# Performance work log

Measured on AMD Instinct MI355X. Metric: run time of the kernel, lower is better.

Reference implementation:

```python
import jax, jax.numpy as jnp
import numpy as np
import math

H = 12
DH = 64
MAX_POS = 1024

def setup_inputs() -> dict:
    key = jax.random.key(0)
    ks = jax.random.split(key, 8)
    B, L, D = 2, 1024, 768
    s = 0.02
    return {
        "hidden_states": jax.random.normal(ks[0], (B, L, D), jnp.float32),
        "attention_mask": jnp.zeros((B, 1, 1, L), jnp.float32),
        "struct_matrix": jax.random.uniform(ks[1], (5, B, 1, L, L), jnp.float32),
        "Wq": jax.random.normal(ks[2], (D, D), jnp.float32) * s,
        "bq": jnp.zeros((D,), jnp.float32),
        "Wk": jax.random.normal(ks[3], (D, D), jnp.float32) * s,
        "bk": jnp.zeros((D,), jnp.float32),
        "Wv": jax.random.normal(ks[4], (D, D), jnp.float32) * s,
        "bv": jnp.zeros((D,), jnp.float32),
        "dist_emb": jax.random.normal(ks[5], (2 * MAX_POS - 1, DH), jnp.float32) * s,
        "ssan_w": jax.random.normal(ks[6], (5, H, DH, DH), jnp.float32) * s,
        "abs_bias": jnp.zeros((5, H), jnp.float32),
    }

def reference(hidden_states, attention_mask, struct_matrix, Wq, bq, Wk, bk, Wv, bv, dist_emb, ssan_w, abs_bias):
    B, L, D = hidden_states.shape

    def heads(x):  # [B,L,D] -> [B,H,L,dh]
        return x.reshape(B, L, H, DH).transpose(0, 2, 1, 3)

    q = heads(hidden_states @ Wq + bq)
    k = heads(hidden_states @ Wk + bk)
    v = heads(hidden_states @ Wv + bv)

    scores = jnp.einsum('bhqd,bhkd->bhqk', q, k)

    # relative_key_query positional scores
    pos_ids = jnp.arange(L)
    distance = pos_ids[:, None] - pos_ids[None, :]          # [L,L]
    pos = dist_emb[distance + MAX_POS - 1]                  # [L,L,dh]
    scores = scores + jnp.einsum('bhld,lrd->bhlr', q, pos)
    scores = scores + jnp.einsum('bhrd,lrd->bhlr', k, pos)

    scores = scores / math.sqrt(DH)
    scores = scores + attention_mask

    # 5 SSAN bilinear bias terms, masked by structural matrices
    for i in range(5):
        bias = jnp.einsum('bhqd,hde,bhke->bhqk', q, ssan_w[i], k)
        scores = scores + (bias + abs_bias[i][None, :, None, None]) * struct_matrix[i]

    probs = jax.nn.softmax(scores, axis=-1)
    ctx = jnp.einsum('bhqk,bhkd->bqhd', probs, v).reshape(B, L, D)
    return ctx
```

## Files before the change

kernel.cpp:

```cpp
#include <hip/hip_runtime.h>
#include <math.h>

#define NB 2
#define NL 1024
#define ND 768
#define NH 12
#define DH 64

typedef _Float16 f16;
typedef _Float16 f16x2 __attribute__((ext_vector_type(2)));
typedef _Float16 f16x4 __attribute__((ext_vector_type(4)));
typedef _Float16 f16x8 __attribute__((ext_vector_type(8)));
typedef float f32x4 __attribute__((ext_vector_type(4)));

#define MFMA16(a, b, c) __builtin_amdgcn_mfma_f32_16x16x32_f16((a), (b), (c), 0, 0, 0)

__device__ __forceinline__ void soft_barrier() {
    asm volatile("s_waitcnt lgkmcnt(0)\n\ts_barrier" ::: "memory");
}

__global__ __launch_bounds__(256) void prep_kernel(
    const float* __restrict__ Wq, const float* __restrict__ Wk,
    const float* __restrict__ Wv, const float* __restrict__ sw,
    const float* __restrict__ de,
    f16* __restrict__ wt, f16* __restrict__ swt, f16* __restrict__ de16)
{
    __shared__ float sT[64 * 66];
    const int t = threadIdx.x;
    const int tile = blockIdx.x;

    if (tile >= 492) {
        const int base = (tile - 492) * 2048 + t * 8;
        if (base < 2047 * 64) {
            float4 a = *(const float4*)&de[base];
            float4 b = *(const float4*)&de[base + 4];
            f16x8 hv;
            hv[0] = (f16)a.x; hv[1] = (f16)a.y; hv[2] = (f16)a.z; hv[3] = (f16)a.w;
            hv[4] = (f16)b.x; hv[5] = (f16)b.y; hv[6] = (f16)b.z; hv[7] = (f16)b.w;
            *(f16x8*)&de16[base] = hv;
        }
        return;
    }

    const float* S; f16* D; int sRS, dRS;
    if (tile < 432) {
        const int mat = tile / 144, r2 = tile % 144, ht = r2 / 12, kt = r2 % 12;
        const float* W = (mat == 0) ? Wq : (mat == 1) ? Wk : Wv;
        S = W + (size_t)(kt * 64) * ND + ht * 64;
        D = wt + (size_t)((mat * NH + ht) * 64) * ND + kt * 64;
        sRS = ND; dRS = ND;
    } else {
        const int i = tile - 432;
        S = sw + (size_t)i * 4096;
        D = swt + (size_t)i * 4096;
        sRS = 64; dRS = 64;
    }

    {
        const int kk = t >> 2, nb = (t & 3) * 16;
        float v[16];
        #pragma unroll
        for (int j = 0; j < 4; ++j)
            *(float4*)&v[4 * j] = *(const float4*)&S[(size_t)kk * sRS + nb + 4 * j];
        #pragma unroll
        for (int jj = 0; jj < 16; ++jj)
            sT[(nb + jj) * 66 + kk] = v[jj];
    }
    soft_barrier();
    {
        const int n = t >> 2, kb = (t & 3) * 16;
        f16 tmp[16];
        #pragma unroll
        for (int j = 0; j < 8; ++j) {
            float2 x = *(float2*)&sT[n * 66 + kb + 2 * j];
            tmp[2 * j]     = (f16)x.x;
            tmp[2 * j + 1] = (f16)x.y;
        }
        *(f16x8*)&D[(size_t)n * dRS + kb]     = *(f16x8*)&tmp[0];
        *(f16x8*)&D[(size_t)n * dRS + kb + 8] = *(f16x8*)&tmp[8];
    }
}

__global__ __launch_bounds__(256, 4) void qkv_kernel(
    const float* __restrict__ hs, const f16* __restrict__ wt,
    const float* __restrict__ bq, const float* __restrict__ bk,
    const float* __restrict__ bv,
    f16* __restrict__ qf, f16* __restrict__ kf, f16* __restrict__ vt)
{
    __shared__ f16 sA[64 * 72], sB[64 * 72];
    __shared__ float sT[64 * 66];

    const int m0  = blockIdx.x * 64;
    const int y   = blockIdx.y;
    const int mat = y / NH, h = y % NH;
    const int t = threadIdx.x, lane = t & 63, w = t >> 6;
    const int quad = lane >> 4, l15 = lane & 15;
    const int wm = w >> 1, wn = w & 1;

    const float* bias = (mat == 0) ? bq : (mat == 1) ? bk : bv;

    f32x4 acc[2][2];
    #pragma unroll
    for (int r = 0; r < 2; ++r)
        #pragma unroll
        for (int c = 0; c < 2; ++c) acc[r][c] = (f32x4){0.f, 0.f, 0.f, 0.f};

    const int srow = t >> 2, scol = (t & 3) * 16;
    const float* Ag = hs + (size_t)(m0 + srow) * ND + scol;
    const f16* Bg = wt + ((size_t)y * 64 + srow) * ND + scol;

    for (int k0 = 0; k0 < ND; k0 += 64) {
        soft_barrier();
        {
            float4 a0 = *(const float4*)&Ag[k0];
            float4 a1 = *(const float4*)&Ag[k0 + 4];
            float4 a2 = *(const float4*)&Ag[k0 + 8];
            float4 a3 = *(const float4*)&Ag[k0 + 12];
            f16x8 ha, hb;
            ha[0] = (f16)a0.x; ha[1] = (f16)a0.y; ha[2] = (f16)a0.z; ha[3] = (f16)a0.w;
            ha[4] = (f16)a1.x; ha[5] = (f16)a1.y; ha[6] = (f16)a1.z; ha[7] = (f16)a1.w;
            hb[0] = (f16)a2.x; hb[1] = (f16)a2.y; hb[2] = (f16)a2.z; hb[3] = (f16)a2.w;
            hb[4] = (f16)a3.x; hb[5] = (f16)a3.y; hb[6] = (f16)a3.z; hb[7] = (f16)a3.w;
            *(f16x8*)&sA[srow * 72 + scol]     = ha;
            *(f16x8*)&sA[srow * 72 + scol + 8] = hb;
        }
        *(f16x8*)&sB[srow * 72 + scol]     = *(const f16x8*)&Bg[k0];
        *(f16x8*)&sB[srow * 72 + scol + 8] = *(const f16x8*)&Bg[k0 + 8];
        soft_barrier();
        #pragma unroll
        for (int kk = 0; kk < 64; kk += 32) {
            const int ko = kk + quad * 8;
            f16x8 a0 = *(f16x8*)&sA[(32 * wm + l15) * 72 + ko];
            f16x8 a1 = *(f16x8*)&sA[(32 * wm + 16 + l15) * 72 + ko];
            f16x8 b0 = *(f16x8*)&sB[(32 * wn + l15) * 72 + ko];
            f16x8 b1 = *(f16x8*)&sB[(32 * wn + 16 + l15) * 72 + ko];
            acc[0][0] = MFMA16(a0, b0, acc[0][0]);
            acc[0][1] = MFMA16(a0, b1, acc[0][1]);
            acc[1][0] = MFMA16(a1, b0, acc[1][0]);
            acc[1][1] = MFMA16(a1, b1, acc[1][1]);
        }
    }
    soft_barrier();

    const int bb = m0 >> 10;
    const int lbase = m0 & 1023;
    const int bh = bb * NH + h;

    if (mat < 2) {
        #pragma unroll
        for (int r = 0; r < 2; ++r)
            #pragma unroll
            for (int c = 0; c < 2; ++c) {
                const int col = 32 * wn + 16 * c + l15;
                const float bz = bias[h * 64 + col];
                #pragma unroll
                for (int rr = 0; rr < 4; ++rr)
                    sT[(32 * wm + 16 * r + 4 * quad + rr) * 66 + col] = acc[r][c][rr] + bz;
            }
        soft_barrier();
        const int orow = t >> 2, ocb = (t & 3) * 16;
        f16 tmp[16];
        #pragma unroll
        for (int j = 0; j < 8; ++j) {
            float2 x = *(float2*)&sT[orow * 66 + ocb + 2 * j];
            tmp[2 * j] = (f16)x.x; tmp[2 * j + 1] = (f16)x.y;
        }
        f16* dst = ((mat == 0) ? qf : kf) + ((size_t)bh * NL + lbase + orow) * DH + ocb;
        *(f16x8*)dst       = *(f16x8*)&tmp[0];
        *(f16x8*)(dst + 8) = *(f16x8*)&tmp[8];
    } else {
        #pragma unroll
        for (int r = 0; r < 2; ++r)
            #pragma unroll
            for (int c = 0; c < 2; ++c) {
                const int col = 32 * wn + 16 * c + l15;
                const float bz = bias[h * 64 + col];
                #pragma unroll
                for (int rr = 0; rr < 4; ++rr)
                    sT[col * 66 + 32 * wm + 16 * r + 4 * quad + rr] = acc[r][c][rr] + bz;
            }
        soft_barrier();
        const int d = t >> 2, lcb = (t & 3) * 16;
        f16 tmp[16];
        #pragma unroll
        for (int j = 0; j < 8; ++j) {
            float2 x = *(float2*)&sT[d * 66 + lcb + 2 * j];
            tmp[2 * j] = (f16)x.x; tmp[2 * j + 1] = (f16)x.y;
        }
        f16* dst = vt + ((size_t)bh * DH + d) * NL + lbase + lcb;
        *(f16x8*)dst       = *(f16x8*)&tmp[0];
        *(f16x8*)(dst + 8) = *(f16x8*)&tmp[8];
    }
}

__global__ __launch_bounds__(256, 2) void attn_kernel(
    const f16* __restrict__ qf, const f16* __restrict__ kf,
    const f16* __restrict__ vt, const f16* __restrict__ swt,
    const float* __restrict__ mask, const float* __restrict__ struct_m,
    const f16* __restrict__ de16, const float* __restrict__ abs_bias,
    float* __restrict__ out)
{
    __shared__ f16 sK[64 * 72];
    __shared__ f16 sVt[2][64 * 72];
    __shared__ f16 sE[96 * 72];
    __shared__ f16 sQEl[96 * 34];
    __shared__ f16 sKEl[96 * 34];
    __shared__ float sS[32 * 68];
    __shared__ f16 sP[32 * 72];
    __shared__ float sAlpha[32], sL[32];

    const int l0 = blockIdx.x * 32;
    const int bh = blockIdx.y;
    const int bb = bh / NH, h = bh % NH;
    const int t  = threadIdx.x;
    const int lane  = t & 63;
    const int w     = t >> 6;
    const int quad  = lane >> 4;
    const int l15   = lane & 15;
    const int msub  = w >> 1;
    const int npair = w & 1;

    f16x8 aQ[2], aW[5][2];
    {
        const size_t qrow = ((size_t)bh * NL + l0 + 16 * msub + l15) * DH;
        #pragma unroll
        for (int K = 0; K < 2; ++K)
            aQ[K] = *(const f16x8*)&qf[qrow + 32 * K + 8 * quad];
    }

    {
        #pragma unroll
        for (int b = 0; b < 2; ++b) {
            const int pb0  = (b == 0) ? 0 : 3;
            const int pcnt = (b == 0) ? 3 : 2;
            #pragma unroll
            for (int pi = 0; pi < 3; ++pi) {
                if (pi < pcnt) {
                    const int p = pb0 + pi;
                    const f16* Wp = swt + ((size_t)(p * NH + h)) * 64 * 64;
                    #pragma unroll
                    for (int ntl = 0; ntl < 2; ++ntl) {
                        const int nt = 2 * npair + ntl;
                        f32x4 c = (f32x4){0.f, 0.f, 0.f, 0.f};
                        #pragma unroll
                        for (int K = 0; K < 2; ++K) {
                            f16x8 bw = *(const f16x8*)&Wp[(size_t)(16 * nt + l15) * 64 + 32 * K + 8 * quad];
                            c = MFMA16(aQ[K], bw, c);
                        }
                        #pragma unroll
                        for (int r = 0; r < 4; ++r)
                            sE[(pi * 32 + 16 * msub + 4 * quad + r) * 72 + 16 * nt + l15] = (f16)c[r];
                    }
                }
            }
            soft_barrier();
            #pragma unroll
            for (int pi = 0; pi < 3; ++pi) {
                if (pi < pcnt) {
                    #pragma unroll
                    for (int K = 0; K < 2; ++K)
                        aW[pb0 + pi][K] =
                            *(const f16x8*)&sE[(pi * 32 + 16 * msub + l15) * 72 + 32 * K + 8 * quad];
                }
            }
            soft_barrier();
        }
    }

    float ab[5];
    #pragma unroll
    for (int p = 0; p < 5; ++p) ab[p] = abs_bias[p * NH + h];

    float pf_st[5][2][4], pf_mask[2];
    f16x8 kreg[2], vreg[2], ereg[3];

    auto issue_kv = [&](int r0s) {
        const int row = t >> 3, col = (t & 7) * 8;
        const f16* ks = kf + ((size_t)bh * NL + r0s) * DH;
        kreg[0] = *(const f16x8*)&ks[row * 64 + col];
        kreg[1] = *(const f16x8*)&ks[(row + 32) * 64 + col];
        const f16* vs = vt + (size_t)bh * DH * NL + r0s;
        vreg[0] = *(const f16x8*)&vs[(size_t)row * NL + col];
        vreg[1] = *(const f16x8*)&vs[(size_t)(row + 32) * NL + col];
    };
    auto write_kv = [&](int buf) {
        const int row = t >> 3, col = (t & 7) * 8;
        *(f16x8*)&sK[row * 72 + col]             = kreg[0];
        *(f16x8*)&sK[(row + 32) * 72 + col]      = kreg[1];
        *(f16x8*)&sVt[buf][row * 72 + col]       = vreg[0];
        *(f16x8*)&sVt[buf][(row + 32) * 72 + col] = vreg[1];
    };
    auto issue_E = [&](int r0s) {
        const int ebase = l0 - r0s + 960;
        #pragma unroll
        for (int p2 = 0; p2 < 3; ++p2) {
            const int idx = t + 256 * p2;
            const int er = idx >> 3, colE = (idx & 7) * 8;
            if (er < 95)
                ereg[p2] = *(const f16x8*)&de16[(size_t)(ebase + er) * DH + colE];
        }
    };
    auto write_E = [&]() {
        #pragma unroll
        for (int p2 = 0; p2 < 3; ++p2) {
            const int idx = t + 256 * p2;
            const int er = idx >> 3, colE = (idx & 7) * 8;
            if (er < 95)
                *(f16x8*)&sE[er * 72 + colE] = ereg[p2];
        }
    };
    auto prefetch = [&](int r0s) {
        #pragma unroll
        for (int n = 0; n < 2; ++n) {
            const int j = 32 * npair + 16 * n + l15;
            pf_mask[n] = mask[bb * NL + r0s + j];
            #pragma unroll
            for (int r = 0; r < 4; ++r) {
                const int i = 16 * msub + 4 * quad + r;
                #pragma unroll
                for (int p = 0; p < 5; ++p)
                    pf_st[p][n][r] =
                        struct_m[((size_t)(p * NB + bb) * NL + l0 + i) * NL + r0s + j];
            }
        }
    };

    issue_kv(0);
    issue_E(0);
    write_kv(0);
    write_E();
    prefetch(0);

    const int sm_i = t >> 3;
    const int sm_jb = t & 7;
    float m_cur = -INFINITY, l_cur = 0.f;
    f32x4 O[2];
    O[0] = (f32x4){0.f, 0.f, 0.f, 0.f};
    O[1] = (f32x4){0.f, 0.f, 0.f, 0.f};

    soft_barrier();

    for (int kt = 0; kt < 16; ++kt) {
        const int cur = kt & 1;

        {
            const int krow = (16 * w + l15) * 72;
            f16x8 ak0 = *(f16x8*)&sK[krow + quad * 8];
            f16x8 ak1 = *(f16x8*)&sK[krow + 32 + quad * 8];
            #pragma unroll
            for (int c = 0; c < 3; ++c) {
                const int nt = 3 - w + c;
                const int erow = (16 * nt + l15) * 72;
                f16x8 e0 = *(f16x8*)&sE[erow + quad * 8];
                f16x8 e1 = *(f16x8*)&sE[erow + 32 + quad * 8];
                f32x4 ck = (f32x4){0.f, 0.f, 0.f, 0.f};
                ck = MFMA16(ak0, e0, ck);
                ck = MFMA16(ak1, e1, ck);
                const int base = (16 * nt + l15) * 34 + 16 * w + 4 * quad;
                f16x2 lo = {(f16)ck[0], (f16)ck[1]};
                f16x2 hi = {(f16)ck[2], (f16)ck[3]};
                *(f16x2*)&sKEl[base]     = lo;
                *(f16x2*)&sKEl[base + 2] = hi;
            }
            const int qs = 3 * npair + msub;
            const int qc = 3 - npair;
            #pragma unroll
            for (int c = 0; c < 3; ++c) {
                if (c < qc) {
                    const int nt = qs + c;
                    const int erow = (16 * nt + l15) * 72;
                    f16x8 e0 = *(f16x8*)&sE[erow + quad * 8];
                    f16x8 e1 = *(f16x8*)&sE[erow + 32 + quad * 8];
                    f32x4 cq = (f32x4){0.f, 0.f, 0.f, 0.f};
                    cq = MFMA16(aQ[0], e0, cq);
                    cq = MFMA16(aQ[1], e1, cq);
                    const int base = (16 * nt + l15) * 34 + 16 * msub + 4 * quad;
                    f16x2 lo = {(f16)cq[0], (f16)cq[1]};
                    f16x2 hi = {(f16)cq[2], (f16)cq[3]};
                    *(f16x2*)&sQEl[base]     = lo;
                    *(f16x2*)&sQEl[base + 2] = hi;
                }
            }
        }
        soft_barrier();

        {
            if (kt < 15) {
                issue_kv((kt + 1) * 64);
                issue_E((kt + 1) * 64);
            }

            f32x4 acc[2][6];
            #pragma unroll
            for (int n = 0; n < 2; ++n)
                #pragma unroll
                for (int p = 0; p < 6; ++p)
                    acc[n][p] = (f32x4){0.f, 0.f, 0.f, 0.f};

            #pragma unroll
            for (int K = 0; K < 2; ++K) {
                const int koff = K * 32 + quad * 8;
                f16x8 bk2[2];
                #pragma unroll
                for (int n = 0; n < 2; ++n)
                    bk2[n] = *(f16x8*)&sK[(32 * npair + 16 * n + l15) * 72 + koff];
                #pragma unroll
                for (int n = 0; n < 2; ++n)
                    acc[n][0] = MFMA16(aQ[K], bk2[n], acc[n][0]);
                #pragma unroll
                for (int p = 0; p < 5; ++p)
                    #pragma unroll
                    for (int n = 0; n < 2; ++n)
                        acc[n][1 + p] = MFMA16(aW[p][K], bk2[n], acc[n][1 + p]);
            }

            #pragma unroll
            for (int n = 0; n < 2; ++n) {
                const int j = 32 * npair + 16 * n + l15;
                #pragma unroll
                for (int r = 0; r < 4; ++r) {
                    const int i = 16 * msub + 4 * quad + r;
                    const int tp = i - j + 63;
                    float posv = (float)sQEl[tp * 34 + i] + (float)sKEl[tp * 34 + j];
                    float s = (acc[n][0][r] + posv) * 0.125f + pf_mask[n];
                    #pragma unroll
                    for (int p = 0; p < 5; ++p)
                        s += (acc[n][1 + p][r] + ab[p]) * pf_st[p][n][r];
                    sS[i * 68 + j] = s;
                }
            }
        }
        soft_barrier();

        {
            float sv[8];
            float smax = -INFINITY;
            #pragma unroll
            for (int k = 0; k < 8; ++k) {
                sv[k] = sS[sm_i * 68 + sm_jb + 8 * k];
                smax = fmaxf(smax, sv[k]);
            }
            #pragma unroll
            for (int off = 4; off > 0; off >>= 1)
                smax = fmaxf(smax, __shfl_xor(smax, off, 8));
            const float m_new = fmaxf(m_cur, smax);
            const float alpha = __expf(m_cur - m_new);
            float rsum = 0.f;
            #pragma unroll
            for (int k = 0; k < 8; ++k) {
                float p = __expf(sv[k] - m_new);
                sP[sm_i * 72 + sm_jb + 8 * k] = (f16)p;
                rsum += p;
            }
            #pragma unroll
            for (int off = 4; off > 0; off >>= 1)
                rsum += __shfl_xor(rsum, off, 8);
            l_cur = l_cur * alpha + rsum;
            m_cur = m_new;
            if (sm_jb == 0) { sAlpha[sm_i] = alpha; sL[sm_i] = l_cur; }

            if (kt < 15) {
                write_kv(cur ^ 1);
                write_E();
                prefetch((kt + 1) * 64);
            }
        }
        soft_barrier();

        {
            float a4[4];
            #pragma unroll
            for (int r = 0; r < 4; ++r) a4[r] = sAlpha[16 * msub + 4 * quad + r];
            #pragma unroll
            for (int n = 0; n < 2; ++n)
                #pragma unroll
                for (int r = 0; r < 4; ++r) O[n][r] *= a4[r];

            const int prow = (16 * msub + l15) * 72;
            #pragma unroll
            for (int K = 0; K < 2; ++K) {
                const int koff = K * 32 + quad * 8;
                f16x8 pfr = *(f16x8*)&sP[prow + koff];
                #pragma unroll
                for (int n = 0; n < 2; ++n) {
                    f16x8 vfr = *(f16x8*)&sVt[cur][(32 * npair + 16 * n + l15) * 72 + koff];
                    O[n] = MFMA16(pfr, vfr, O[n]);
                }
            }
        }
    }

    float linv[4];
    #pragma unroll
    for (int r = 0; r < 4; ++r) linv[r] = 1.0f / sL[16 * msub + 4 * quad + r];
    #pragma unroll
    for (int n = 0; n < 2; ++n) {
        const int dh = 32 * npair + 16 * n + l15;
        #pragma unroll
        for (int r = 0; r < 4; ++r) {
            const int i = 16 * msub + 4 * quad + r;
            out[((size_t)bb * NL + l0 + i) * ND + h * DH + dh] = O[n][r] * linv[r];
        }
    }
}

extern "C" void kernel_launch(void* const* d_in, const int* in_sizes, int n_in,
                              void* d_out, int out_size, void* d_ws, size_t ws_size,
                              hipStream_t stream) {
    const float* hs   = (const float*)d_in[0];
    const float* mask = (const float*)d_in[1];
    const float* stm  = (const float*)d_in[2];
    const float* Wq   = (const float*)d_in[3];
    const float* bq   = (const float*)d_in[4];
    const float* Wk   = (const float*)d_in[5];
    const float* bk   = (const float*)d_in[6];
    const float* Wv   = (const float*)d_in[7];
    const float* bv   = (const float*)d_in[8];
    const float* de   = (const float*)d_in[9];
    const float* sw   = (const float*)d_in[10];
    const float* abb  = (const float*)d_in[11];
    float* outp = (float*)d_out;

    const size_t NQKV = (size_t)NB * NH * NL * DH;
    char* ws = (char*)d_ws;
    f16* qf   = (f16*)ws;                 ws += NQKV * 2;
    f16* kf   = (f16*)ws;                 ws += NQKV * 2;
    f16* vtb  = (f16*)ws;                 ws += NQKV * 2;
    f16* wt   = (f16*)ws;                 ws += (size_t)2304 * 768 * 2;
    f16* swt  = (f16*)ws;                 ws += (size_t)245760 * 2;
    f16* de16 = (f16*)ws;

    prep_kernel<<<556, 256, 0, stream>>>(Wq, Wk, Wv, sw, de, wt, swt, de16);
    qkv_kernel<<<dim3(32, 36), 256, 0, stream>>>(hs, wt, bq, bk, bv, qf, kf, vtb);
    attn_kernel<<<dim3(32, 24), 256, 0, stream>>>(qf, kf, vtb, swt,
                                                  mask, stm, de16, abb, outp);
}
```

Baseline: 220.0 us.

## Retile QKV GEMM to 128x128 with double-buffered LDS and pre-converted fp16 input

The hidden-states fp32-to-fp16 conversion moves into the prep kernel, so the QKV GEMM reads fp16 activations directly. The QKV kernel switches from 64x64 to 128x128 tiles with a 4x4 MFMA grid per wave, which raises data reuse. It also double-buffers LDS, prefetching the next K-slice into registers while computing the current one. The cost is higher register and LDS pressure, lower occupancy (launch bounds 2), a grid of only 288 blocks, and an extra fp16 copy of the input in workspace.

```diff
diff --git a/kernel.cpp b/kernel.cpp
--- a/kernel.cpp
+++ b/kernel.cpp
@@ -20,17 +20,29 @@
 }
 
 __global__ __launch_bounds__(256) void prep_kernel(
+    const float* __restrict__ hs,
     const float* __restrict__ Wq, const float* __restrict__ Wk,
     const float* __restrict__ Wv, const float* __restrict__ sw,
     const float* __restrict__ de,
-    f16* __restrict__ wt, f16* __restrict__ swt, f16* __restrict__ de16)
+    f16* __restrict__ hsf, f16* __restrict__ wt, f16* __restrict__ swt,
+    f16* __restrict__ de16)
 {
     __shared__ float sT[64 * 66];
     const int t = threadIdx.x;
     const int tile = blockIdx.x;
 
-    if (tile >= 492) {
-        const int base = (tile - 492) * 2048 + t * 8;
+    if (tile < 768) {
+        const int base = tile * 2048 + t * 8;
+        float4 a = *(const float4*)&hs[base];
+        float4 b = *(const float4*)&hs[base + 4];
+        f16x8 hv;
+        hv[0] = (f16)a.x; hv[1] = (f16)a.y; hv[2] = (f16)a.z; hv[3] = (f16)a.w;
+        hv[4] = (f16)b.x; hv[5] = (f16)b.y; hv[6] = (f16)b.z; hv[7] = (f16)b.w;
+        *(f16x8*)&hsf[base] = hv;
+        return;
+    }
+    if (tile >= 1260) {
+        const int base = (tile - 1260) * 2048 + t * 8;
         if (base < 2047 * 64) {
             float4 a = *(const float4*)&de[base];
             float4 b = *(const float4*)&de[base + 4];
@@ -43,14 +55,15 @@
     }
 
     const float* S; f16* D; int sRS, dRS;
-    if (tile < 432) {
-        const int mat = tile / 144, r2 = tile % 144, ht = r2 / 12, kt = r2 % 12;
+    const int ti = tile - 768;
+    if (ti < 432) {
+        const int mat = ti / 144, r2 = ti % 144, ht = r2 / 12, kt = r2 % 12;
         const float* W = (mat == 0) ? Wq : (mat == 1) ? Wk : Wv;
         S = W + (size_t)(kt * 64) * ND + ht * 64;
         D = wt + (size_t)((mat * NH + ht) * 64) * ND + kt * 64;
         sRS = ND; dRS = ND;
     } else {
-        const int i = tile - 432;
+        const int i = ti - 432;
         S = sw + (size_t)i * 4096;
         D = swt + (size_t)i * 4096;
         sRS = 64; dRS = 64;
@@ -81,115 +94,122 @@
     }
 }
 
-__global__ __launch_bounds__(256, 4) void qkv_kernel(
-    const float* __restrict__ hs, const f16* __restrict__ wt,
+__global__ __launch_bounds__(256, 2) void qkv_kernel(
+    const f16* __restrict__ hsf, const f16* __restrict__ wt,
     const float* __restrict__ bq, const float* __restrict__ bk,
     const float* __restrict__ bv,
     f16* __restrict__ qf, f16* __restrict__ kf, f16* __restrict__ vt)
 {
-    __shared__ f16 sA[64 * 72], sB[64 * 72];
-    __shared__ float sT[64 * 66];
-
-    const int m0  = blockIdx.x * 64;
-    const int y   = blockIdx.y;
-    const int mat = y / NH, h = y % NH;
+    __shared__ f16 sAB[2][2][128 * 72];
+
+    const int m0 = blockIdx.x * 128;
+    const int n0 = blockIdx.y * 128;
+    const int mat = n0 / 768;
+    const int h0  = (n0 % 768) / 64;
+    const int bb  = m0 >> 10;
+    const int l0  = m0 & 1023;
+
     const int t = threadIdx.x, lane = t & 63, w = t >> 6;
     const int quad = lane >> 4, l15 = lane & 15;
     const int wm = w >> 1, wn = w & 1;
 
     const float* bias = (mat == 0) ? bq : (mat == 1) ? bk : bv;
 
-    f32x4 acc[2][2];
-    #pragma unroll
-    for (int r = 0; r < 2; ++r)
-        #pragma unroll
-        for (int c = 0; c < 2; ++c) acc[r][c] = (f32x4){0.f, 0.f, 0.f, 0.f};
-
-    const int srow = t >> 2, scol = (t & 3) * 16;
-    const float* Ag = hs + (size_t)(m0 + srow) * ND + scol;
-    const f16* Bg = wt + ((size_t)y * 64 + srow) * ND + scol;
-
-    for (int k0 = 0; k0 < ND; k0 += 64) {
+    const int srow = t >> 1;
+    const int scol = (t & 1) * 32;
+    const f16* Ag = hsf + (size_t)(m0 + srow) * ND + scol;
+    const f16* Bg = wt  + (size_t)(n0 + srow) * ND + scol;
+
+    f16x8 ar[4], br[4];
+    f32x4 acc[4][4];
+    #pragma unroll
+    for (int mi = 0; mi < 4; ++mi)
+        #pragma unroll
+        for (int ni = 0; ni < 4; ++ni)
+            acc[mi][ni] = (f32x4){0.f, 0.f, 0.f, 0.f};
+
+    #pragma unroll
+    for (int j = 0; j < 4; ++j) {
+        ar[j] = *(const f16x8*)&Ag[8 * j];
+        br[j] = *(const f16x8*)&Bg[8 * j];
+    }
+    #pragma unroll
+    for (int j = 0; j < 4; ++j) {
+        *(f16x8*)&sAB[0][0][srow * 72 + scol + 8 * j] = ar[j];
+        *(f16x8*)&sAB[0][1][srow * 72 + scol + 8 * j] = br[j];
+    }
+
+    for (int kt2 = 0; kt2 < 12; ++kt2) {
+        const int cur = kt2 & 1;
         soft_barrier();
-        {
-            float4 a0 = *(const float4*)&Ag[k0];
-            float4 a1 = *(const float4*)&Ag[k0 + 4];
-            float4 a2 = *(const float4*)&Ag[k0 + 8];
-            float4 a3 = *(const float4*)&Ag[k0 + 12];
-            f16x8 ha, hb;
-            ha[0] = (f16)a0.x; ha[1] = (f16)a0.y; ha[2] = (f16)a0.z; ha[3] = (f16)a0.w;
-            ha[4] = (f16)a1.x; ha[5] = (f16)a1.y; ha[6] = (f16)a1.z; ha[7] = (f16)a1.w;
-            hb[0] = (f16)a2.x; hb[1] = (f16)a2.y; hb[2] = (f16)a2.z; hb[3] = (f16)a2.w;
-            hb[4] = (f16)a3.x; hb[5] = (f16)a3.y; hb[6] = (f16)a3.z; hb[7] = (f16)a3.w;
-            *(f16x8*)&sA[srow * 72 + scol]     = ha;
-            *(f16x8*)&sA[srow * 72 + scol + 8] = hb;
-        }
-        *(f16x8*)&sB[srow * 72 + scol]     = *(const f16x8*)&Bg[k0];
-        *(f16x8*)&sB[srow * 72 + scol + 8] = *(const f16x8*)&Bg[k0 + 8];
-        soft_barrier();
+        if (kt2 < 11) {
+            const int k0 = (kt2 + 1) * 64;
+            #pragma unroll
+            for (int j = 0; j < 4; ++j) {
+                ar[j] = *(const f16x8*)&Ag[k0 + 8 * j];
+                br[j] = *(const f16x8*)&Bg[k0 + 8 * j];
+            }
+        }
         #pragma unroll
         for (int kk = 0; kk < 64; kk += 32) {
             const int ko = kk + quad * 8;
-            f16x8 a0 = *(f16x8*)&sA[(32 * wm + l15) * 72 + ko];
-            f16x8 a1 = *(f16x8*)&sA[(32 * wm + 16 + l15) * 72 + ko];
-            f16x8 b0 = *(f16x8*)&sB[(32 * wn + l15) * 72 + ko];
-            f16x8 b1 = *(f16x8*)&sB[(32 * wn + 16 + l15) * 72 + ko];
-            acc[0][0] = MFMA16(a0, b0, acc[0][0]);
-            acc[0][1] = MFMA16(a0, b1, acc[0][1]);
-            acc[1][0] = MFMA16(a1, b0, acc[1][0]);
-            acc[1][1] = MFMA16(a1, b1, acc[1][1]);
+            f16x8 af[4], bf[4];
+            #pragma unroll
+            for (int i = 0; i < 4; ++i) {
+                af[i] = *(f16x8*)&sAB[cur][0][(64 * wm + 16 * i + l15) * 72 + ko];
+                bf[i] = *(f16x8*)&sAB[cur][1][(64 * wn + 16 * i + l15) * 72 + ko];
+            }
+            #pragma unroll
+            for (int mi = 0; mi < 4; ++mi)
+                #pragma unroll
+                for (int ni = 0; ni < 4; ++ni)
+                    acc[mi][ni] = MFMA16(af[mi], bf[ni], acc[mi][ni]);
+        }
+        if (kt2 < 11) {
+            #pragma unroll
+            for (int j = 0; j < 4; ++j) {
+                *(f16x8*)&sAB[cur ^ 1][0][srow * 72 + scol + 8 * j] = ar[j];
+                *(f16x8*)&sAB[cur ^ 1][1][srow * 72 + scol + 8 * j] = br[j];
+            }
         }
     }
     soft_barrier();
 
-    const int bb = m0 >> 10;
-    const int lbase = m0 & 1023;
-    const int bh = bb * NH + h;
+    f16* sC = (f16*)sAB;
+    float bz[4];
+    #pragma unroll
+    for (int ni = 0; ni < 4; ++ni)
+        bz[ni] = bias[(n0 % 768) + 64 * wn + 16 * ni + l15];
+
+    #pragma unroll
+    for (int mi = 0; mi < 4; ++mi)
+        #pragma unroll
+        for (int ni = 0; ni < 4; ++ni) {
+            const int col = 64 * wn + 16 * ni + l15;
+            #pragma unroll
+            for (int r = 0; r < 4; ++r) {
+                const int row = 64 * wm + 16 * mi + 4 * quad + r;
+                const f16 v = (f16)(acc[mi][ni][r] + bz[ni]);
+                if (mat == 2) sC[col * 136 + row] = v;
+                else          sC[row * 136 + col] = v;
+            }
+        }
+    soft_barrier();
 
     if (mat < 2) {
-        #pragma unroll
-        for (int r = 0; r < 2; ++r)
-            #pragma unroll
-            for (int c = 0; c < 2; ++c) {
-                const int col = 32 * wn + 16 * c + l15;
-                const float bz = bias[h * 64 + col];
-                #pragma unroll
-                for (int rr = 0; rr < 4; ++rr)
-                    sT[(32 * wm + 16 * r + 4 * quad + rr) * 66 + col] = acc[r][c][rr] + bz;
-            }
-        soft_barrier();
-        const int orow = t >> 2, ocb = (t & 3) * 16;
-        f16 tmp[16];
-        #pragma unroll
-        for (int j = 0; j < 8; ++j) {
-            float2 x = *(float2*)&sT[orow * 66 + ocb + 2 * j];
-            tmp[2 * j] = (f16)x.x; tmp[2 * j + 1] = (f16)x.y;
-        }
-        f16* dst = ((mat == 0) ? qf : kf) + ((size_t)bh * NL + lbase + orow) * DH + ocb;
-        *(f16x8*)dst       = *(f16x8*)&tmp[0];
-        *(f16x8*)(dst + 8) = *(f16x8*)&tmp[8];
+        const int row = t >> 1, half = t & 1;
+        f16* dst = ((mat == 0) ? qf : kf)
+                 + ((size_t)(bb * NH + h0 + half) * NL + l0 + row) * DH;
+        #pragma unroll
+        for (int j = 0; j < 8; ++j)
+            *(f16x8*)&dst[8 * j] = *(f16x8*)&sC[row * 136 + 64 * half + 8 * j];
     } else {
-        #pragma unroll
-        for (int r = 0; r < 2; ++r)
-            #pragma unroll
-            for (int c = 0; c < 2; ++c) {
-                const int col = 32 * wn + 16 * c + l15;
-                const float bz = bias[h * 64 + col];
-                #pragma unroll
-                for (int rr = 0; rr < 4; ++rr)
-                    sT[col * 66 + 32 * wm + 16 * r + 4 * quad + rr] = acc[r][c][rr] + bz;
-            }
-        soft_barrier();
-        const int d = t >> 2, lcb = (t & 3) * 16;
-        f16 tmp[16];
-        #pragma unroll
-        for (int j = 0; j < 8; ++j) {
-            float2 x = *(float2*)&sT[d * 66 + lcb + 2 * j];
-            tmp[2 * j] = (f16)x.x; tmp[2 * j + 1] = (f16)x.y;
-        }
-        f16* dst = vt + ((size_t)bh * DH + d) * NL + lbase + lcb;
-        *(f16x8*)dst       = *(f16x8*)&tmp[0];
-        *(f16x8*)(dst + 8) = *(f16x8*)&tmp[8];
+        const int c = t >> 1, half = t & 1;
+        const int d = c & 63, hh = h0 + (c >> 6);
+        f16* dst = vt + ((size_t)(bb * NH + hh) * DH + d) * NL + l0 + 64 * half;
+        #pragma unroll
+        for (int j = 0; j < 8; ++j)
+            *(f16x8*)&dst[8 * j] = *(f16x8*)&sC[c * 136 + 64 * half + 8 * j];
     }
 }
 
@@ -526,12 +546,14 @@
     f16* qf   = (f16*)ws;                 ws += NQKV * 2;
     f16* kf   = (f16*)ws;                 ws += NQKV * 2;
     f16* vtb  = (f16*)ws;                 ws += NQKV * 2;
+    f16* hsf  = (f16*)ws;                 ws += NQKV * 2;
     f16* wt   = (f16*)ws;                 ws += (size_t)2304 * 768 * 2;
     f16* swt  = (f16*)ws;                 ws += (size_t)245760 * 2;
     f16* de16 = (f16*)ws;
 
-    prep_kernel<<<556, 256, 0, stream>>>(Wq, Wk, Wv, sw, de, wt, swt, de16);
-    qkv_kernel<<<dim3(32, 36), 256, 0, stream>>>(hs, wt, bq, bk, bv, qf, kf, vtb);
+    prep_kernel<<<1324, 256, 0, stream>>>(hs, Wq, Wk, Wv, sw, de,
+                                          hsf, wt, swt, de16);
+    qkv_kernel<<<dim3(16, 18), 256, 0, stream>>>(hsf, wt, bq, bk, bv, qf, kf, vtb);
     attn_kernel<<<dim3(32, 24), 256, 0, stream>>>(qf, kf, vtb, swt,
                                                   mask, stm, de16, abb, outp);
 }
```

Result: no change. 218.3 us (-0.8%).
